# Performance work log

Measured on AMD Instinct MI355X. Metric: run time of the kernel, lower is better.

The kernel has to match this reference:

```python
import jax, jax.numpy as jnp
import numpy as np

B, S = 2, 2048
DIM_IN, DIM_OUT, NUM_HEADS, DIM_QK = 1024, 128, 16, 128


def setup_inputs() -> dict:
    key = jax.random.key(0)
    k0, k1, k2, k3 = jax.random.split(key, 4)
    x = jax.random.normal(k0, (B, S, DIM_IN), jnp.float32)
    mask = jax.random.bernoulli(k1, 0.1, (B, S))  # True = masked-out token
    # xavier-normal-ish scales (exact init values are irrelevant for correctness)
    std_in = float(np.sqrt(2.0 / (NUM_HEADS * DIM_QK + DIM_IN * DIM_QK)))
    proj_in = jax.random.normal(k2, (DIM_IN, NUM_HEADS, 2 * DIM_QK + DIM_OUT), jnp.float32) * std_in
    v_bias = jnp.zeros((NUM_HEADS, DIM_OUT), jnp.float32)
    std_out = float(np.sqrt(2.0 / (DIM_OUT * DIM_OUT + NUM_HEADS * DIM_OUT)))
    proj_out = jax.random.normal(k3, (NUM_HEADS, DIM_OUT, DIM_OUT), jnp.float32) * std_out
    proj_out_bias = jnp.zeros((DIM_OUT,), jnp.float32)
    return {"x": x, "mask": mask, "proj_in": proj_in, "v_bias": v_bias,
            "proj_out": proj_out, "proj_out_bias": proj_out_bias}


def _rotary(t):
    # t: [z, s, h, d]; GPT-NeoX style rotary as in the torch Rotary module
    d = t.shape[-1]
    half = -(-d // 2)  # ceil(d/2), matches torch.arange(0,-1,-2/d)
    freq_half = 10000.0 ** (jnp.arange(half, dtype=jnp.float32) * (-2.0 / d))
    freq = jnp.concatenate([freq_half, freq_half[: half - d % 2]])  # length d
    pos = jnp.arange(t.shape[1], dtype=jnp.float32)
    ang = pos[:, None] * freq[None, :]             # [s, d]
    cos = jnp.cos(ang)[None, :, None, :]
    sin = jnp.sin(ang)[None, :, None, :]
    x1, x2 = jnp.split(t, 2, axis=-1)
    rot = jnp.concatenate([-x2, x1], axis=-1)
    return t * cos + rot * sin


def _inf_cube(t):
    return t ** 3


def reference(x, mask, proj_in, v_bias, proj_out, proj_out_bias):
    qkv = jnp.einsum('zki,iho->zkho', x, proj_in)
    q, k, v = jnp.split(qkv, [DIM_QK, 2 * DIM_QK], axis=-1)
    q = _rotary(q)
    k = _rotary(k)
    scores = jnp.einsum('zqha,zkha->zqkh', q, k) / jnp.sqrt(jnp.float32(DIM_QK))
    # dual mask: row (query) OR column (key) masked -> -inf
    m = jnp.logical_or(mask[:, :, None, None], mask[:, None, :, None])  # [z,q,k,1]
    scores = jnp.where(m, -jnp.inf, scores)
    attn = jnp.nan_to_num(jax.nn.softmax(scores, axis=2))  # softmax over k; nan rows -> 0
    o = jnp.einsum('zqkh,zkhx->zqhx', attn, v + v_bias[None, None])
    out = jnp.einsum('zqhx,hxy->zqy', _inf_cube(o), proj_out) + proj_out_bias[None, None]
    return _inf_cube(out)
```

## Files before the change

### kernel.cpp

```cpp
#include <hip/hip_runtime.h>
#include <math.h>

#define BZ 2
#define SQ 2048
#define DIN 1024
#define HH 16
#define NT 6144
#define MROWS 4096
#define KOUT 2048
#define KSPLIT 8

typedef unsigned short u16t;
typedef unsigned int u32t;
typedef __attribute__((ext_vector_type(8))) short bf16x8;
typedef __attribute__((ext_vector_type(4))) float f32x4;

__device__ __forceinline__ float cubef(float x) { return x * x * x; }

__device__ __forceinline__ u16t f2bf(float f) {
    u32t b = __float_as_uint(f);
    b += 0x7FFFu + ((b >> 16) & 1u);
    return (u16t)(b >> 16);
}
__device__ __forceinline__ float bf2f(u16t u) { return __uint_as_float(((u32t)u) << 16); }
__device__ __forceinline__ u32t pk2(float a, float b) {
    return (u32t)f2bf(a) | ((u32t)f2bf(b) << 16);
}

#if __has_builtin(__builtin_amdgcn_exp2f)
#define EXP2(x) __builtin_amdgcn_exp2f(x)
#else
#define EXP2(x) exp2f(x)
#endif

__device__ __forceinline__ void load_lds16(const void* g, void* l) {
    __builtin_amdgcn_global_load_lds((const __attribute__((address_space(1))) void*)g,
                                     (__attribute__((address_space(3))) void*)l, 16, 0, 0);
}

__global__ __launch_bounds__(256) void bf16_x(const float* __restrict__ x,
                                              u16t* __restrict__ xb) {
    const size_t idx = ((size_t)blockIdx.x * 256 + threadIdx.x) * 8;
    float4 f0 = *(const float4*)&x[idx];
    float4 f1 = *(const float4*)&x[idx + 4];
    u32t h[4];
    h[0] = pk2(f0.x, f0.y); h[1] = pk2(f0.z, f0.w);
    h[2] = pk2(f1.x, f1.y); h[3] = pk2(f1.z, f1.w);
    *(uint4*)&xb[idx] = *(uint4*)&h[0];
}

__global__ __launch_bounds__(256) void rope_table(float* __restrict__ tab) {
    const int idx = blockIdx.x * 256 + threadIdx.x;
    const int s = idx >> 6, d = idx & 63;
    float f = expf(-0.14391156831212788f * (float)d);
    float sn, cs;
    sincosf((float)s * f, &sn, &cs);
    ((float2*)tab)[idx] = make_float2(cs, sn);
}

__global__ __launch_bounds__(256) void transpose_w(const float* __restrict__ W,
                                                   u16t* __restrict__ Th) {
    __shared__ float tile[64][68];
    const int n0 = blockIdx.x * 64;
    const int k0 = blockIdx.y * 64;
    const int t = threadIdx.x;
    {
        const int r = t >> 4, c = (t & 15) * 4;
        #pragma unroll
        for (int p = 0; p < 4; p++) {
            float4 v = *(const float4*)&W[(size_t)(k0 + r + p * 16) * NT + n0 + c];
            *(float4*)&tile[r + p * 16][c] = v;
        }
    }
    __syncthreads();
    const int nr = t >> 2;
    const int kc = (t & 3) * 16;
    u32t hi[8];
    #pragma unroll
    for (int j = 0; j < 8; j++)
        hi[j] = pk2(tile[kc + 2 * j][nr], tile[kc + 2 * j + 1][nr]);
    size_t ob = (size_t)(n0 + nr) * DIN + k0 + kc;
    *(uint4*)&Th[ob]     = *(uint4*)&hi[0];
    *(uint4*)&Th[ob + 8] = *(uint4*)&hi[4];
}

__global__ __launch_bounds__(256) void transpose_w2(const float* __restrict__ W,
                                                    u16t* __restrict__ Th) {
    __shared__ float tile[64][68];
    const int n0 = blockIdx.x * 64;
    const int k0 = blockIdx.y * 64;
    const int t = threadIdx.x;
    {
        const int r = t >> 4, c = (t & 15) * 4;
        #pragma unroll
        for (int p = 0; p < 4; p++) {
            float4 v = *(const float4*)&W[(size_t)(k0 + r + p * 16) * 128 + n0 + c];
            *(float4*)&tile[r + p * 16][c] = v;
        }
    }
    __syncthreads();
    const int nr = t >> 2;
    const int kc = (t & 3) * 16;
    u32t hi[8];
    #pragma unroll
    for (int j = 0; j < 8; j++)
        hi[j] = pk2(tile[kc + 2 * j][nr], tile[kc + 2 * j + 1][nr]);
    size_t ob = (size_t)(n0 + nr) * KOUT + k0 + kc;
    *(uint4*)&Th[ob]     = *(uint4*)&hi[0];
    *(uint4*)&Th[ob + 8] = *(uint4*)&hi[4];
}

#define QSC 0.12751744f

#define GQ_STAGE(TI) do {                                                  \
    const int _k0 = (TI) * 32;                                             \
    const int _bb = ((TI) & 3) * 8192;                                     \
    load_lds16(aPtr + _k0,     &smem[_bb + wbase]);                        \
    load_lds16(aPtr + _k0 + 8, &smem[_bb + wbase + 1024]);                 \
    load_lds16(bPtr + _k0,     &smem[_bb + 4096 + wbase]);                 \
    load_lds16(bPtr + _k0 + 8, &smem[_bb + 4096 + wbase + 1024]);          \
} while (0)

#define GQ_COMPUTE(TI) do {                                                \
    const int _bb = ((TI) & 3) * 8192;                                     \
    bf16x8 ah[4], bh[4];                                                   \
    _Pragma("unroll")                                                      \
    for (int mt = 0; mt < 4; mt++)                                         \
        ah[mt] = *(const bf16x8*)&smem[_bb + quad * 1024 + (wm + mt * 16 + l15) * 8]; \
    _Pragma("unroll")                                                      \
    for (int nt = 0; nt < 4; nt++)                                         \
        bh[nt] = *(const bf16x8*)&smem[_bb + 4096 + quad * 1024 + (wn + nt * 16 + l15) * 8]; \
    __builtin_amdgcn_s_setprio(1);                                         \
    _Pragma("unroll")                                                      \
    for (int mt = 0; mt < 4; mt++)                                         \
        _Pragma("unroll")                                                  \
        for (int nt = 0; nt < 4; nt++)                                     \
            acc[mt][nt] = __builtin_amdgcn_mfma_f32_16x16x32_bf16(ah[mt], bh[nt], acc[mt][nt], 0, 0, 0); \
    __builtin_amdgcn_s_setprio(0);                                         \
} while (0)

#define GQ_WAITBAR(N) do {                                                 \
    asm volatile("s_waitcnt vmcnt(" #N ")" ::: "memory");                  \
    __builtin_amdgcn_s_barrier();                                          \
    __builtin_amdgcn_sched_barrier(0);                                     \
} while (0)

__global__ __launch_bounds__(256, 2) void gemm_qkv6(const u16t* __restrict__ Ah,
                                                    const u16t* __restrict__ Bh,
                                                    const float* __restrict__ vb,
                                                    const float* __restrict__ ropetab,
                                                    u16t* __restrict__ QB,
                                                    u16t* __restrict__ KB,
                                                    u16t* __restrict__ VTh) {
    __shared__ __align__(16) u16t smem[32768];

    const int t = threadIdx.x;
    const int lane = t & 63, wid = t >> 6;
    const int quad = lane >> 4, l15 = lane & 15;
    const int wm = (wid & 1) * 64;
    const int wn = (wid >> 1) * 64;

    const int f = blockIdx.y * 48 + blockIdx.x;
    const int L = (f & 7) * 192 + (f >> 3);
    const int rect = L / 48, rrem = L - rect * 48;
    const int tileI = (rect & 7) * 6 + rrem % 6;
    const int rowIdx = (rect >> 3) * 8 + rrem / 6;
    const int h = tileI / 3, t3 = tileI - h * 3;
    const int colBase = tileI * 128;
    const int rowBase = rowIdx * 128;
    const int sm = t & 127;
    const int skh = t >> 7;

    f32x4 acc[4][4];
    #pragma unroll
    for (int i = 0; i < 4; i++)
        #pragma unroll
        for (int j = 0; j < 4; j++) acc[i][j] = (f32x4){0.f, 0.f, 0.f, 0.f};

    const u16t* aPtr = Ah + (size_t)(rowBase + sm) * DIN + skh * 16;
    const u16t* bPtr = Bh + (size_t)(colBase + sm) * DIN + skh * 16;
    const int wbase = (wid >> 1) * 2048 + (wid & 1) * 512;

    GQ_STAGE(0);
    GQ_STAGE(1);
    for (int i = 0; i < 30; i++) {
        GQ_STAGE(i + 2);
        GQ_WAITBAR(8);
        GQ_COMPUTE(i);
    }
    GQ_WAITBAR(4);
    GQ_COMPUTE(30);
    GQ_WAITBAR(0);
    GQ_COMPUTE(31);
    __syncthreads();

    const int z = rowBase >> 11;
    const int s0local = rowBase & 2047;
    const size_t zh = (size_t)(z * 16 + h);
    u16t* tl = smem;

    if (t3 == 2) {
        #pragma unroll
        for (int nt = 0; nt < 4; nt++) {
            float bbv = vb[h * 128 + wn + nt * 16 + l15];
            #pragma unroll
            for (int mt = 0; mt < 4; mt++)
                #pragma unroll
                for (int r = 0; r < 4; r++)
                    tl[(wm + mt * 16 + quad * 4 + r) * 136 + wn + nt * 16 + l15] =
                        f2bf(acc[mt][nt][r] + bbv);
        }
    } else {
        #pragma unroll
        for (int nt = 0; nt < 4; nt++)
            #pragma unroll
            for (int mt = 0; mt < 4; mt++)
                #pragma unroll
                for (int r = 0; r < 4; r++)
                    tl[(wm + mt * 16 + quad * 4 + r) * 136 + wn + nt * 16 + l15] =
                        f2bf(acc[mt][nt][r]);
    }
    __syncthreads();

    if (t3 != 2) {
        u16t* dstQK = (t3 ? KB : QB) + zh * 262144;
        const float sc = t3 ? 1.0f : QSC;
        const int rr = t >> 2;
        const int ch = (t & 3) << 4;
        #pragma unroll
        for (int half = 0; half < 2; half++) {
            const int row = rr + half * 64;
            const int s = s0local + row;
            const u16t* trow = &tl[row * 136];
            uint4 X1  = *(const uint4*)&trow[ch];
            uint4 X1b = *(const uint4*)&trow[ch + 8];
            uint4 X2  = *(const uint4*)&trow[ch + 64];
            uint4 X2b = *(const uint4*)&trow[ch + 72];
            u32t A_[8] = {X1.x, X1.y, X1.z, X1.w, X1b.x, X1b.y, X1b.z, X1b.w};
            u32t B_[8] = {X2.x, X2.y, X2.z, X2.w, X2b.x, X2b.y, X2b.z, X2b.w};
            u32t OA[8], OB[8];
            const float4* tb = (const float4*)&ropetab[(size_t)s * 128 + ch * 2];
            #pragma unroll
            for (int p = 0; p < 8; p++) {
                float4 tt = tb[p];
                float cs0 = tt.x * sc, sn0 = tt.y * sc;
                float cs1 = tt.z * sc, sn1 = tt.w * sc;
                float x1a = bf2f((u16t)(A_[p] & 0xFFFFu)), x1b = bf2f((u16t)(A_[p] >> 16));
                float x2a = bf2f((u16t)(B_[p] & 0xFFFFu)), x2b = bf2f((u16t)(B_[p] >> 16));
                OA[p] = pk2(x1a * cs0 - x2a * sn0, x1b * cs1 - x2b * sn1);
                OB[p] = pk2(x2a * cs0 + x1a * sn0, x2b * cs1 + x1b * sn1);
            }
            u16t* d0 = dstQK + (size_t)s * 128 + ch;
            *(uint4*)d0        = make_uint4(OA[0], OA[1], OA[2], OA[3]);
            *(uint4*)(d0 + 8)  = make_uint4(OA[4], OA[5], OA[6], OA[7]);
            *(uint4*)(d0 + 64) = make_uint4(OB[0], OB[1], OB[2], OB[3]);
            *(uint4*)(d0 + 72) = make_uint4(OB[4], OB[5], OB[6], OB[7]);
        }
    } else {
        u16t* dstV = VTh + zh * 262144 + (size_t)(s0local >> 5) * 4096;
        const int d = t & 127;
        const int g0 = t >> 7;
        #pragma unroll
        for (int gg = 0; gg < 2; gg++) {
            const int g = g0 + 2 * gg;
            const u16t* col = &tl[(g * 32) * 136 + d];
            u32t H[16];
            #pragma unroll
            for (int m = 0; m < 16; m++) {
                u32t lo = col[m * 136];
                u32t hi = col[(m + 16) * 136];
                H[m] = lo | (hi << 16);
            }
            u16t* dv = dstV + (size_t)g * 4096 + d * 32;
            *(uint4*)&dv[0]  = *(uint4*)&H[0];
            *(uint4*)&dv[8]  = *(uint4*)&H[4];
            *(uint4*)&dv[16] = *(uint4*)&H[8];
            *(uint4*)&dv[24] = *(uint4*)&H[12];
        }
    }
}

__global__ __launch_bounds__(256, 2) void attn_kernel9(const u16t* __restrict__ QB,
                                                       const u16t* __restrict__ KB,
                                                       const u16t* __restrict__ VTh,
                                                       const int* __restrict__ mask,
                                                       u16t* __restrict__ O3b) {
    const int blk = blockIdx.x;
    const int qt = blk & 15;
    const int h  = (blk >> 4) & 15;
    const int z  = blk >> 8;
    const int t  = threadIdx.x;
    const int lane = t & 63, wid = t >> 6;
    const int quad = lane >> 4, l15 = lane & 15;

    __shared__ __align__(16) u16t ks[2][32 * 136];
    __shared__ __align__(16) u16t vth[2][128 * 40];
    __shared__ __align__(16) u16t wlb[128 * 40];
    __shared__ int km[2][32];

    const int q0 = qt * 128;
    const size_t zh = (size_t)(z * 16 + h);
    const u16t* qb  = QB  + zh * 262144;
    const u16t* kb  = KB  + zh * 262144;
    const u16t* vhg = VTh + zh * 262144;

    bf16x8 qf[2][4];
    #pragma unroll
    for (int i = 0; i < 2; i++)
        #pragma unroll
        for (int kk = 0; kk < 4; kk++)
            qf[i][kk] = *(const bf16x8*)(qb + (size_t)(q0 + 16 * (2 * wid + i) + l15) * 128 + kk * 32 + quad * 8);

    int4 qm4[2];
    #pragma unroll
    for (int i = 0; i < 2; i++)
        qm4[i] = *(const int4*)&mask[z * SQ + q0 + 16 * (2 * wid + i) + 4 * quad];
    const int qmr[2][4] = {{qm4[0].x, qm4[0].y, qm4[0].z, qm4[0].w},
                           {qm4[1].x, qm4[1].y, qm4[1].z, qm4[1].w}};
    int rowoff[2];
    #pragma unroll
    for (int i = 0; i < 2; i++) rowoff[i] = (16 * (2 * wid + i) + 4 * quad) * 40;

    const int srow = t >> 3, sco = (t & 7) * 16;
    const int sdd = t >> 1, sk0 = (t & 1) * 16;

    uint4 ka, kb2, va, vb2;
    int kmv = 0;
    {
        ka  = *(const uint4*)(kb + t * 16);
        kb2 = *(const uint4*)(kb + t * 16 + 8);
        va  = *(const uint4*)(vhg + t * 16);
        vb2 = *(const uint4*)(vhg + t * 16 + 8);
        if (t < 32) kmv = mask[z * SQ + t];
    }

    f32x4 acc[2][8];
    #pragma unroll
    for (int i = 0; i < 2; i++)
        #pragma unroll
        for (int d = 0; d < 8; d++) acc[i][d] = (f32x4){0.f, 0.f, 0.f, 0.f};
    float dsum[2][4] = {{0.f, 0.f, 0.f, 0.f}, {0.f, 0.f, 0.f, 0.f}};

    for (int it = 0; it < 64; it++) {
        const int buf = it & 1;
        *(uint4*)&ks[buf][srow * 136 + sco]     = ka;
        *(uint4*)&ks[buf][srow * 136 + sco + 8] = kb2;
        *(uint4*)&vth[buf][sdd * 40 + sk0]      = va;
        *(uint4*)&vth[buf][sdd * 40 + sk0 + 8]  = vb2;
        if (t < 32) km[buf][t] = kmv;

        __syncthreads();

        {
            const int ktn = (it < 63) ? (it + 1) * 32 : it * 32;
            const u16t* src = kb + (size_t)ktn * 128 + t * 16;
            ka  = *(const uint4*)(src);
            kb2 = *(const uint4*)(src + 8);
            const u16t* srch = vhg + (size_t)(ktn >> 5) * 4096 + t * 16;
            va  = *(const uint4*)(srch);
            vb2 = *(const uint4*)(srch + 8);
            if (t < 32) kmv = mask[z * SQ + ktn + t];
        }

        f32x4 s4[2][2];
        #pragma unroll
        for (int i = 0; i < 2; i++)
            #pragma unroll
            for (int n = 0; n < 2; n++) s4[i][n] = (f32x4){0.f, 0.f, 0.f, 0.f};
        __builtin_amdgcn_s_setprio(1);
        #pragma unroll
        for (int kk = 0; kk < 4; kk++) {
            bf16x8 kf0 = *(const bf16x8*)&ks[buf][l15 * 136 + kk * 32 + quad * 8];
            bf16x8 kf1 = *(const bf16x8*)&ks[buf][(16 + l15) * 136 + kk * 32 + quad * 8];
            s4[0][0] = __builtin_amdgcn_mfma_f32_16x16x32_bf16(qf[0][kk], kf0, s4[0][0], 0, 0, 0);
            s4[0][1] = __builtin_amdgcn_mfma_f32_16x16x32_bf16(qf[0][kk], kf1, s4[0][1], 0, 0, 0);
            s4[1][0] = __builtin_amdgcn_mfma_f32_16x16x32_bf16(qf[1][kk], kf0, s4[1][0], 0, 0, 0);
            s4[1][1] = __builtin_amdgcn_mfma_f32_16x16x32_bf16(qf[1][kk], kf1, s4[1][1], 0, 0, 0);
        }
        __builtin_amdgcn_s_setprio(0);
        {
            int colm0 = km[buf][l15], colm1 = km[buf][16 + l15];
            #pragma unroll
            for (int i = 0; i < 2; i++)
                #pragma unroll
                for (int r = 0; r < 4; r++) {
                    float w0 = colm0 ? 0.f : EXP2(s4[i][0][r]);
                    float w1 = colm1 ? 0.f : EXP2(s4[i][1][r]);
                    dsum[i][r] += w0 + w1;
                    u32t pkw;
                    asm("v_cvt_pk_bf16_f32 %0, %1, %2" : "=v"(pkw) : "v"(w0), "v"(w1));
                    *(u32t*)&wlb[rowoff[i] + r * 40 + 2 * l15] = pkw;
                }
        }
        bf16x8 pa[2];
        #pragma unroll
        for (int i = 0; i < 2; i++)
            pa[i] = *(const bf16x8*)&wlb[(16 * (2 * wid + i) + l15) * 40 + quad * 8];
        __builtin_amdgcn_s_setprio(1);
        #pragma unroll
        for (int dt = 0; dt < 8; dt++) {
            bf16x8 vh = *(const bf16x8*)&vth[buf][(16 * dt + l15) * 40 + quad * 8];
            acc[0][dt] = __builtin_amdgcn_mfma_f32_16x16x32_bf16(pa[0], vh, acc[0][dt], 0, 0, 0);
            acc[1][dt] = __builtin_amdgcn_mfma_f32_16x16x32_bf16(pa[1], vh, acc[1][dt], 0, 0, 0);
        }
        __builtin_amdgcn_s_setprio(0);
    }

    #pragma unroll
    for (int i = 0; i < 2; i++)
        #pragma unroll
        for (int r = 0; r < 4; r++) {
            float v = dsum[i][r];
            v += __shfl_xor(v, 1);
            v += __shfl_xor(v, 2);
            v += __shfl_xor(v, 4);
            v += __shfl_xor(v, 8);
            dsum[i][r] = v;
        }

    #pragma unroll
    for (int i = 0; i < 2; i++)
        #pragma unroll
        for (int r = 0; r < 4; r++) {
            int row = 16 * (2 * wid + i) + 4 * quad + r;
            float inv = (qmr[i][r] || !(dsum[i][r] > 0.f)) ? 0.f : 1.f / dsum[i][r];
            u16t* dst = O3b + (size_t)(z * SQ + q0 + row) * KOUT + h * 128;
            #pragma unroll
            for (int dt = 0; dt < 8; dt++)
                dst[16 * dt + l15] = f2bf(cubef(acc[i][dt][r] * inv));
        }
}

__global__ __launch_bounds__(256, 2) void final_gemm4(const u16t* __restrict__ Ab,
                                                      const u16t* __restrict__ Bh,
                                                      float* __restrict__ part) {
    __shared__ __align__(16) u16t smem[32768];

    const int t = threadIdx.x;
    const int lane = t & 63, wid = t >> 6;
    const int quad = lane >> 4, l15 = lane & 15;
    const int wm = (wid & 1) * 64;
    const int wn = (wid >> 1) * 64;
    const int rowBase = blockIdx.x * 128;
    const int kBase   = blockIdx.y * (KOUT / KSPLIT);
    const int sm = t & 127;
    const int skh = t >> 7;

    f32x4 acc[4][4];
    #pragma unroll
    for (int i = 0; i < 4; i++)
        #pragma unroll
        for (int j = 0; j < 4; j++) acc[i][j] = (f32x4){0.f, 0.f, 0.f, 0.f};

    const u16t* aPtr = Ab + (size_t)(rowBase + sm) * KOUT + kBase + skh * 16;
    const u16t* bPtr = Bh + (size_t)sm * KOUT + kBase + skh * 16;
    const int wbase = (wid >> 1) * 2048 + (wid & 1) * 512;

    GQ_STAGE(0);
    GQ_STAGE(1);
    for (int i = 0; i < 6; i++) {
        GQ_STAGE(i + 2);
        GQ_WAITBAR(8);
        GQ_COMPUTE(i);
    }
    GQ_WAITBAR(4);
    GQ_COMPUTE(6);
    GQ_WAITBAR(0);
    GQ_COMPUTE(7);

    float* pbase = part + (size_t)blockIdx.y * ((size_t)MROWS * 128);
    #pragma unroll
    for (int mt = 0; mt < 4; mt++)
        #pragma unroll
        for (int nt = 0; nt < 4; nt++) {
            int col = wn + nt * 16 + l15;
            #pragma unroll
            for (int r = 0; r < 4; r++) {
                int row = rowBase + wm + mt * 16 + quad * 4 + r;
                pbase[(size_t)row * 128 + col] = acc[mt][nt][r];
            }
        }
}

__global__ __launch_bounds__(256) void reduce_bias_cube(const float* __restrict__ part,
                                                        const float* __restrict__ bias,
                                                        float* __restrict__ out) {
    const int idx = (blockIdx.x * 256 + threadIdx.x) * 4;
    float4 s = {0.f, 0.f, 0.f, 0.f};
    #pragma unroll
    for (int p = 0; p < KSPLIT; p++) {
        float4 v = *(const float4*)&part[(size_t)p * ((size_t)MROWS * 128) + idx];
        s.x += v.x; s.y += v.y; s.z += v.z; s.w += v.w;
    }
    float4 b = *(const float4*)&bias[idx & 127];
    float4 r;
    r.x = cubef(s.x + b.x);
    r.y = cubef(s.y + b.y);
    r.z = cubef(s.z + b.z);
    r.w = cubef(s.w + b.w);
    *(float4*)&out[idx] = r;
}

extern "C" void kernel_launch(void* const* d_in, const int* in_sizes, int n_in,
                              void* d_out, int out_size, void* d_ws, size_t ws_size,
                              hipStream_t stream) {
    const float* x        = (const float*)d_in[0];
    const int*   mask     = (const int*)d_in[1];
    const float* proj_in  = (const float*)d_in[2];
    const float* v_bias   = (const float*)d_in[3];
    const float* proj_out = (const float*)d_in[4];
    const float* po_bias  = (const float*)d_in[5];
    float* out = (float*)d_out;

    u16t* QB  = (u16t*)d_ws;
    u16t* KB  = QB + (size_t)8388608;
    u16t* VTh = KB + (size_t)8388608;
    u16t* xb  = VTh + (size_t)8388608;
    u16t* O3b = xb + (size_t)4194304;
    u16t* pTh = O3b;
    float* ropetab = (float*)(O3b + (size_t)6291456);
    u16t* WTh = QB;
    float* partials = (float*)(WTh + (size_t)128 * KOUT);

    bf16_x<<<(MROWS * DIN) / (256 * 8), 256, 0, stream>>>(x, xb);
    rope_table<<<(SQ * 64) / 256, 256, 0, stream>>>(ropetab);
    transpose_w<<<dim3(NT / 64, DIN / 64), 256, 0, stream>>>(proj_in, pTh);
    gemm_qkv6<<<dim3(48, MROWS / 128), 256, 0, stream>>>(xb, pTh, v_bias, ropetab, QB, KB, VTh);
    attn_kernel9<<<BZ * HH * (SQ / 128), 256, 0, stream>>>(QB, KB, VTh, mask, O3b);
    transpose_w2<<<dim3(2, KOUT / 64), 256, 0, stream>>>(proj_out, WTh);
    final_gemm4<<<dim3(MROWS / 128, KSPLIT), 256, 0, stream>>>(O3b, WTh, partials);
    reduce_bias_cube<<<(MROWS * 128) / (256 * 4), 256, 0, stream>>>(partials, po_bias, out);
}
```

Baseline: 300.6 us.

## Merge prep kernels into one launch and use register-prefetch QKV GEMM

Three preprocessing kernels (x to bf16, rope table, proj_in transpose) become a single launch that picks its branch by block index, removing two launch gaps. The QKV GEMM moves from a 4-stage global_load_lds pipeline with a 64 KB LDS footprint to a simpler double-buffered version. That version prefetches the next K-tile into registers, stores it to LDS and syncs once per step, using about 34 KB of LDS with no explicit occupancy hint. The attention kernel is only moved within the file. This risks losing the deeper async-copy overlap of the old GEMM in exchange for lower LDS use and fewer launches.

```diff
diff --git a/kernel.cpp b/kernel.cpp
--- a/kernel.cpp
+++ b/kernel.cpp
@@ -38,50 +38,53 @@
                                      (__attribute__((address_space(3))) void*)l, 16, 0, 0);
 }
 
-__global__ __launch_bounds__(256) void bf16_x(const float* __restrict__ x,
-                                              u16t* __restrict__ xb) {
-    const size_t idx = ((size_t)blockIdx.x * 256 + threadIdx.x) * 8;
-    float4 f0 = *(const float4*)&x[idx];
-    float4 f1 = *(const float4*)&x[idx + 4];
-    u32t h[4];
-    h[0] = pk2(f0.x, f0.y); h[1] = pk2(f0.z, f0.w);
-    h[2] = pk2(f1.x, f1.y); h[3] = pk2(f1.z, f1.w);
-    *(uint4*)&xb[idx] = *(uint4*)&h[0];
-}
-
-__global__ __launch_bounds__(256) void rope_table(float* __restrict__ tab) {
-    const int idx = blockIdx.x * 256 + threadIdx.x;
-    const int s = idx >> 6, d = idx & 63;
-    float f = expf(-0.14391156831212788f * (float)d);
-    float sn, cs;
-    sincosf((float)s * f, &sn, &cs);
-    ((float2*)tab)[idx] = make_float2(cs, sn);
-}
-
-__global__ __launch_bounds__(256) void transpose_w(const float* __restrict__ W,
-                                                   u16t* __restrict__ Th) {
+__global__ __launch_bounds__(256) void prep_all(const float* __restrict__ x,
+                                                u16t* __restrict__ xb,
+                                                float* __restrict__ tab,
+                                                const float* __restrict__ W,
+                                                u16t* __restrict__ Th) {
     __shared__ float tile[64][68];
-    const int n0 = blockIdx.x * 64;
-    const int k0 = blockIdx.y * 64;
+    const int bx = blockIdx.x;
     const int t = threadIdx.x;
-    {
-        const int r = t >> 4, c = (t & 15) * 4;
-        #pragma unroll
-        for (int p = 0; p < 4; p++) {
-            float4 v = *(const float4*)&W[(size_t)(k0 + r + p * 16) * NT + n0 + c];
-            *(float4*)&tile[r + p * 16][c] = v;
-        }
-    }
-    __syncthreads();
-    const int nr = t >> 2;
-    const int kc = (t & 3) * 16;
-    u32t hi[8];
-    #pragma unroll
-    for (int j = 0; j < 8; j++)
-        hi[j] = pk2(tile[kc + 2 * j][nr], tile[kc + 2 * j + 1][nr]);
-    size_t ob = (size_t)(n0 + nr) * DIN + k0 + kc;
-    *(uint4*)&Th[ob]     = *(uint4*)&hi[0];
-    *(uint4*)&Th[ob + 8] = *(uint4*)&hi[4];
+
+    if (bx < 2048) {
+        const size_t idx = ((size_t)bx * 256 + t) * 8;
+        float4 f0 = *(const float4*)&x[idx];
+        float4 f1 = *(const float4*)&x[idx + 4];
+        u32t h[4];
+        h[0] = pk2(f0.x, f0.y); h[1] = pk2(f0.z, f0.w);
+        h[2] = pk2(f1.x, f1.y); h[3] = pk2(f1.z, f1.w);
+        *(uint4*)&xb[idx] = *(uint4*)&h[0];
+    } else if (bx < 2560) {
+        const int idx = (bx - 2048) * 256 + t;
+        const int s = idx >> 6, d = idx & 63;
+        float f = expf(-0.14391156831212788f * (float)d);
+        float sn, cs;
+        sincosf((float)s * f, &sn, &cs);
+        ((float2*)tab)[idx] = make_float2(cs, sn);
+    } else {
+        const int idx = bx - 2560;
+        const int n0 = (idx % 96) * 64;
+        const int k0 = (idx / 96) * 64;
+        {
+            const int r = t >> 4, c = (t & 15) * 4;
+            #pragma unroll
+            for (int p = 0; p < 4; p++) {
+                float4 v = *(const float4*)&W[(size_t)(k0 + r + p * 16) * NT + n0 + c];
+                *(float4*)&tile[r + p * 16][c] = v;
+            }
+        }
+        __syncthreads();
+        const int nr = t >> 2;
+        const int kc = (t & 3) * 16;
+        u32t hi[8];
+        #pragma unroll
+        for (int j = 0; j < 8; j++)
+            hi[j] = pk2(tile[kc + 2 * j][nr], tile[kc + 2 * j + 1][nr]);
+        size_t ob = (size_t)(n0 + nr) * DIN + k0 + kc;
+        *(uint4*)&Th[ob]     = *(uint4*)&hi[0];
+        *(uint4*)&Th[ob + 8] = *(uint4*)&hi[4];
+    }
 }
 
 __global__ __launch_bounds__(256) void transpose_w2(const float* __restrict__ W,
@@ -111,6 +114,322 @@
 }
 
 #define QSC 0.12751744f
+
+__global__ __launch_bounds__(256) void gemm_qkv9(const u16t* __restrict__ Ah,
+                                                 const u16t* __restrict__ Bh,
+                                                 const float* __restrict__ vb,
+                                                 const float* __restrict__ ropetab,
+                                                 u16t* __restrict__ QB,
+                                                 u16t* __restrict__ KB,
+                                                 u16t* __restrict__ VTh) {
+    __shared__ __align__(16) u16t smem[17408];
+
+    const int t = threadIdx.x;
+    const int lane = t & 63, wid = t >> 6;
+    const int quad = lane >> 4, l15 = lane & 15;
+    const int wm = (wid & 1) * 64;
+    const int wn = (wid >> 1) * 64;
+
+    const int f = blockIdx.y * 48 + blockIdx.x;
+    const int L = (f & 7) * 192 + (f >> 3);
+    const int rect = L / 48, rrem = L - rect * 48;
+    const int tileI = (rect & 7) * 6 + rrem % 6;
+    const int rowIdx = (rect >> 3) * 8 + rrem / 6;
+    const int h = tileI / 3, t3 = tileI - h * 3;
+    const int colBase = tileI * 128;
+    const int rowBase = rowIdx * 128;
+    const int sm = t & 127;
+    const int skh = t >> 7;
+
+    f32x4 acc[4][4];
+    #pragma unroll
+    for (int i = 0; i < 4; i++)
+        #pragma unroll
+        for (int j = 0; j < 4; j++) acc[i][j] = (f32x4){0.f, 0.f, 0.f, 0.f};
+
+    const u16t* aPtr = Ah + (size_t)(rowBase + sm) * DIN + skh * 16;
+    const u16t* bPtr = Bh + (size_t)(colBase + sm) * DIN + skh * 16;
+    const int swoff = skh * 2048 + sm * 8;
+
+    uint4 a0 = *(const uint4*)(aPtr);
+    uint4 a1 = *(const uint4*)(aPtr + 8);
+    uint4 b0 = *(const uint4*)(bPtr);
+    uint4 b1 = *(const uint4*)(bPtr + 8);
+
+    for (int it = 0; it < 32; it++) {
+        const int buf = it & 1;
+        const int ab = buf * 4096, bb_ = 8192 + buf * 4096;
+        *(uint4*)(&smem[ab + swoff])         = a0;
+        *(uint4*)(&smem[ab + swoff + 1024])  = a1;
+        *(uint4*)(&smem[bb_ + swoff])        = b0;
+        *(uint4*)(&smem[bb_ + swoff + 1024]) = b1;
+        __syncthreads();
+        {
+            const int k0 = (it < 31) ? (it + 1) * 32 : it * 32;
+            a0 = *(const uint4*)(aPtr + k0);
+            a1 = *(const uint4*)(aPtr + k0 + 8);
+            b0 = *(const uint4*)(bPtr + k0);
+            b1 = *(const uint4*)(bPtr + k0 + 8);
+        }
+        bf16x8 ah[4], bh[4];
+        #pragma unroll
+        for (int mt = 0; mt < 4; mt++)
+            ah[mt] = *(const bf16x8*)&smem[ab + quad * 1024 + (wm + mt * 16 + l15) * 8];
+        #pragma unroll
+        for (int nt = 0; nt < 4; nt++)
+            bh[nt] = *(const bf16x8*)&smem[bb_ + quad * 1024 + (wn + nt * 16 + l15) * 8];
+        __builtin_amdgcn_s_setprio(1);
+        #pragma unroll
+        for (int mt = 0; mt < 4; mt++)
+            #pragma unroll
+            for (int nt = 0; nt < 4; nt++)
+                acc[mt][nt] = __builtin_amdgcn_mfma_f32_16x16x32_bf16(ah[mt], bh[nt], acc[mt][nt], 0, 0, 0);
+        __builtin_amdgcn_s_setprio(0);
+    }
+    __syncthreads();
+
+    const int z = rowBase >> 11;
+    const int s0local = rowBase & 2047;
+    const size_t zh = (size_t)(z * 16 + h);
+    u16t* tl = smem;
+
+    if (t3 == 2) {
+        #pragma unroll
+        for (int nt = 0; nt < 4; nt++) {
+            float bbv = vb[h * 128 + wn + nt * 16 + l15];
+            #pragma unroll
+            for (int mt = 0; mt < 4; mt++)
+                #pragma unroll
+                for (int r = 0; r < 4; r++)
+                    tl[(wm + mt * 16 + quad * 4 + r) * 136 + wn + nt * 16 + l15] =
+                        f2bf(acc[mt][nt][r] + bbv);
+        }
+    } else {
+        #pragma unroll
+        for (int nt = 0; nt < 4; nt++)
+            #pragma unroll
+            for (int mt = 0; mt < 4; mt++)
+                #pragma unroll
+                for (int r = 0; r < 4; r++)
+                    tl[(wm + mt * 16 + quad * 4 + r) * 136 + wn + nt * 16 + l15] =
+                        f2bf(acc[mt][nt][r]);
+    }
+    __syncthreads();
+
+    if (t3 != 2) {
+        u16t* dstQK = (t3 ? KB : QB) + zh * 262144;
+        const float sc = t3 ? 1.0f : QSC;
+        const int rr = t >> 2;
+        const int ch = (t & 3) << 4;
+        #pragma unroll
+        for (int half = 0; half < 2; half++) {
+            const int row = rr + half * 64;
+            const int s = s0local + row;
+            const u16t* trow = &tl[row * 136];
+            uint4 X1  = *(const uint4*)&trow[ch];
+            uint4 X1b = *(const uint4*)&trow[ch + 8];
+            uint4 X2  = *(const uint4*)&trow[ch + 64];
+            uint4 X2b = *(const uint4*)&trow[ch + 72];
+            u32t A_[8] = {X1.x, X1.y, X1.z, X1.w, X1b.x, X1b.y, X1b.z, X1b.w};
+            u32t B_[8] = {X2.x, X2.y, X2.z, X2.w, X2b.x, X2b.y, X2b.z, X2b.w};
+            u32t OA[8], OB[8];
+            const float4* tb = (const float4*)&ropetab[(size_t)s * 128 + ch * 2];
+            #pragma unroll
+            for (int p = 0; p < 8; p++) {
+                float4 tt = tb[p];
+                float cs0 = tt.x * sc, sn0 = tt.y * sc;
+                float cs1 = tt.z * sc, sn1 = tt.w * sc;
+                float x1a = bf2f((u16t)(A_[p] & 0xFFFFu)), x1b = bf2f((u16t)(A_[p] >> 16));
+                float x2a = bf2f((u16t)(B_[p] & 0xFFFFu)), x2b = bf2f((u16t)(B_[p] >> 16));
+                OA[p] = pk2(x1a * cs0 - x2a * sn0, x1b * cs1 - x2b * sn1);
+                OB[p] = pk2(x2a * cs0 + x1a * sn0, x2b * cs1 + x1b * sn1);
+            }
+            u16t* d0 = dstQK + (size_t)s * 128 + ch;
+            *(uint4*)d0        = make_uint4(OA[0], OA[1], OA[2], OA[3]);
+            *(uint4*)(d0 + 8)  = make_uint4(OA[4], OA[5], OA[6], OA[7]);
+            *(uint4*)(d0 + 64) = make_uint4(OB[0], OB[1], OB[2], OB[3]);
+            *(uint4*)(d0 + 72) = make_uint4(OB[4], OB[5], OB[6], OB[7]);
+        }
+    } else {
+        u16t* dstV = VTh + zh * 262144 + (size_t)(s0local >> 5) * 4096;
+        const int d = t & 127;
+        const int g0 = t >> 7;
+        #pragma unroll
+        for (int gg = 0; gg < 2; gg++) {
+            const int g = g0 + 2 * gg;
+            const u16t* col = &tl[(g * 32) * 136 + d];
+            u32t H[16];
+            #pragma unroll
+            for (int m = 0; m < 16; m++) {
+                u32t lo = col[m * 136];
+                u32t hi = col[(m + 16) * 136];
+                H[m] = lo | (hi << 16);
+            }
+            u16t* dv = dstV + (size_t)g * 4096 + d * 32;
+            *(uint4*)&dv[0]  = *(uint4*)&H[0];
+            *(uint4*)&dv[8]  = *(uint4*)&H[4];
+            *(uint4*)&dv[16] = *(uint4*)&H[8];
+            *(uint4*)&dv[24] = *(uint4*)&H[12];
+        }
+    }
+}
+
+__global__ __launch_bounds__(256, 2) void attn_kernel9(const u16t* __restrict__ QB,
+                                                       const u16t* __restrict__ KB,
+                                                       const u16t* __restrict__ VTh,
+                                                       const int* __restrict__ mask,
+                                                       u16t* __restrict__ O3b) {
+    const int blk = blockIdx.x;
+    const int qt = blk & 15;
+    const int h  = (blk >> 4) & 15;
+    const int z  = blk >> 8;
+    const int t  = threadIdx.x;
+    const int lane = t & 63, wid = t >> 6;
+    const int quad = lane >> 4, l15 = lane & 15;
+
+    __shared__ __align__(16) u16t ks[2][32 * 136];
+    __shared__ __align__(16) u16t vth[2][128 * 40];
+    __shared__ __align__(16) u16t wlb[128 * 40];
+    __shared__ int km[2][32];
+
+    const int q0 = qt * 128;
+    const size_t zh = (size_t)(z * 16 + h);
+    const u16t* qb  = QB  + zh * 262144;
+    const u16t* kb  = KB  + zh * 262144;
+    const u16t* vhg = VTh + zh * 262144;
+
+    bf16x8 qf[2][4];
+    #pragma unroll
+    for (int i = 0; i < 2; i++)
+        #pragma unroll
+        for (int kk = 0; kk < 4; kk++)
+            qf[i][kk] = *(const bf16x8*)(qb + (size_t)(q0 + 16 * (2 * wid + i) + l15) * 128 + kk * 32 + quad * 8);
+
+    int4 qm4[2];
+    #pragma unroll
+    for (int i = 0; i < 2; i++)
+        qm4[i] = *(const int4*)&mask[z * SQ + q0 + 16 * (2 * wid + i) + 4 * quad];
+    const int qmr[2][4] = {{qm4[0].x, qm4[0].y, qm4[0].z, qm4[0].w},
+                           {qm4[1].x, qm4[1].y, qm4[1].z, qm4[1].w}};
+    int rowoff[2];
+    #pragma unroll
+    for (int i = 0; i < 2; i++) rowoff[i] = (16 * (2 * wid + i) + 4 * quad) * 40;
+
+    const int srow = t >> 3, sco = (t & 7) * 16;
+    const int sdd = t >> 1, sk0 = (t & 1) * 16;
+
+    uint4 ka, kb2, va, vb2;
+    int kmv = 0;
+    {
+        ka  = *(const uint4*)(kb + t * 16);
+        kb2 = *(const uint4*)(kb + t * 16 + 8);
+        va  = *(const uint4*)(vhg + t * 16);
+        vb2 = *(const uint4*)(vhg + t * 16 + 8);
+        if (t < 32) kmv = mask[z * SQ + t];
+    }
+
+    f32x4 acc[2][8];
+    #pragma unroll
+    for (int i = 0; i < 2; i++)
+        #pragma unroll
+        for (int d = 0; d < 8; d++) acc[i][d] = (f32x4){0.f, 0.f, 0.f, 0.f};
+    float dsum[2][4] = {{0.f, 0.f, 0.f, 0.f}, {0.f, 0.f, 0.f, 0.f}};
+
+    for (int it = 0; it < 64; it++) {
+        const int buf = it & 1;
+        *(uint4*)&ks[buf][srow * 136 + sco]     = ka;
+        *(uint4*)&ks[buf][srow * 136 + sco + 8] = kb2;
+        *(uint4*)&vth[buf][sdd * 40 + sk0]      = va;
+        *(uint4*)&vth[buf][sdd * 40 + sk0 + 8]  = vb2;
+        if (t < 32) km[buf][t] = kmv;
+
+        __syncthreads();
+
+        {
+            const int ktn = (it < 63) ? (it + 1) * 32 : it * 32;
+            const u16t* src = kb + (size_t)ktn * 128 + t * 16;
+            ka  = *(const uint4*)(src);
+            kb2 = *(const uint4*)(src + 8);
+            const u16t* srch = vhg + (size_t)(ktn >> 5) * 4096 + t * 16;
+            va  = *(const uint4*)(srch);
+            vb2 = *(const uint4*)(srch + 8);
+            if (t < 32) kmv = mask[z * SQ + ktn + t];
+        }
+
+        f32x4 s4[2][2];
+        #pragma unroll
+        for (int i = 0; i < 2; i++)
+            #pragma unroll
+            for (int n = 0; n < 2; n++) s4[i][n] = (f32x4){0.f, 0.f, 0.f, 0.f};
+        __builtin_amdgcn_s_setprio(1);
+        #pragma unroll
+        for (int kk = 0; kk < 4; kk++) {
+            bf16x8 kf0 = *(const bf16x8*)&ks[buf][l15 * 136 + kk * 32 + quad * 8];
+            bf16x8 kf1 = *(const bf16x8*)&ks[buf][(16 + l15) * 136 + kk * 32 + quad * 8];
+            s4[0][0] = __builtin_amdgcn_mfma_f32_16x16x32_bf16(qf[0][kk], kf0, s4[0][0], 0, 0, 0);
+            s4[0][1] = __builtin_amdgcn_mfma_f32_16x16x32_bf16(qf[0][kk], kf1, s4[0][1], 0, 0, 0);
+            s4[1][0] = __builtin_amdgcn_mfma_f32_16x16x32_bf16(qf[1][kk], kf0, s4[1][0], 0, 0, 0);
+            s4[1][1] = __builtin_amdgcn_mfma_f32_16x16x32_bf16(qf[1][kk], kf1, s4[1][1], 0, 0, 0);
+        }
+        __builtin_amdgcn_s_setprio(0);
+        {
+            int colm0 = km[buf][l15], colm1 = km[buf][16 + l15];
+            #pragma unroll
+            for (int i = 0; i < 2; i++)
+                #pragma unroll
+                for (int r = 0; r < 4; r++) {
+                    float w0 = colm0 ? 0.f : EXP2(s4[i][0][r]);
+                    float w1 = colm1 ? 0.f : EXP2(s4[i][1][r]);
+                    dsum[i][r] += w0 + w1;
+                    u32t pkw;
+                    asm("v_cvt_pk_bf16_f32 %0, %1, %2" : "=v"(pkw) : "v"(w0), "v"(w1));
+                    *(u32t*)&wlb[rowoff[i] + r * 40 + 2 * l15] = pkw;
+                }
+        }
+        bf16x8 pa[2];
+        #pragma unroll
+        for (int i = 0; i < 2; i++)
+            pa[i] = *(const bf16x8*)&wlb[(16 * (2 * wid + i) + l15) * 40 + quad * 8];
+        __builtin_amdgcn_s_setprio(1);
+        #pragma unroll
+        for (int dt = 0; dt < 8; dt++) {
+            bf16x8 vh = *(const bf16x8*)&vth[buf][(16 * dt + l15) * 40 + quad * 8];
+            acc[0][dt] = __builtin_amdgcn_mfma_f32_16x16x32_bf16(pa[0], vh, acc[0][dt], 0, 0, 0);
+            acc[1][dt] = __builtin_amdgcn_mfma_f32_16x16x32_bf16(pa[1], vh, acc[1][dt], 0, 0, 0);
+        }
+        __builtin_amdgcn_s_setprio(0);
+    }
+
+    #pragma unroll
+    for (int i = 0; i < 2; i++)
+        #pragma unroll
+        for (int r = 0; r < 4; r++) {
+            float v = dsum[i][r];
+            v += __shfl_xor(v, 1);
+            v += __shfl_xor(v, 2);
+            v += __shfl_xor(v, 4);
+            v += __shfl_xor(v, 8);
+            dsum[i][r] = v;
+        }
+
+    #pragma unroll
+    for (int i = 0; i < 2; i++)
+        #pragma unroll
+        for (int r = 0; r < 4; r++) {
+            int row = 16 * (2 * wid + i) + 4 * quad + r;
+            float inv = (qmr[i][r] || !(dsum[i][r] > 0.f)) ? 0.f : 1.f / dsum[i][r];
+            u16t* dst = O3b + (size_t)(z * SQ + q0 + row) * KOUT + h * 128;
+            #pragma unroll
+            for (int dt = 0; dt < 8; dt++)
+                dst[16 * dt + l15] = f2bf(cubef(acc[i][dt][r] * inv));
+        }
+}
+
+#define GQ_WAITBAR(N) do {                                                 \
+    asm volatile("s_waitcnt vmcnt(" #N ")" ::: "memory");                  \
+    __builtin_amdgcn_s_barrier();                                          \
+    __builtin_amdgcn_sched_barrier(0);                                     \
+} while (0)
 
 #define GQ_STAGE(TI) do {                                                  \
     const int _k0 = (TI) * 32;                                             \
@@ -139,298 +458,6 @@
     __builtin_amdgcn_s_setprio(0);                                         \
 } while (0)
 
-#define GQ_WAITBAR(N) do {                                                 \
-    asm volatile("s_waitcnt vmcnt(" #N ")" ::: "memory");                  \
-    __builtin_amdgcn_s_barrier();                                          \
-    __builtin_amdgcn_sched_barrier(0);                                     \
-} while (0)
-
-__global__ __launch_bounds__(256, 2) void gemm_qkv6(const u16t* __restrict__ Ah,
-                                                    const u16t* __restrict__ Bh,
-                                                    const float* __restrict__ vb,
-                                                    const float* __restrict__ ropetab,
-                                                    u16t* __restrict__ QB,
-                                                    u16t* __restrict__ KB,
-                                                    u16t* __restrict__ VTh) {
-    __shared__ __align__(16) u16t smem[32768];
-
-    const int t = threadIdx.x;
-    const int lane = t & 63, wid = t >> 6;
-    const int quad = lane >> 4, l15 = lane & 15;
-    const int wm = (wid & 1) * 64;
-    const int wn = (wid >> 1) * 64;
-
-    const int f = blockIdx.y * 48 + blockIdx.x;
-    const int L = (f & 7) * 192 + (f >> 3);
-    const int rect = L / 48, rrem = L - rect * 48;
-    const int tileI = (rect & 7) * 6 + rrem % 6;
-    const int rowIdx = (rect >> 3) * 8 + rrem / 6;
-    const int h = tileI / 3, t3 = tileI - h * 3;
-    const int colBase = tileI * 128;
-    const int rowBase = rowIdx * 128;
-    const int sm = t & 127;
-    const int skh = t >> 7;
-
-    f32x4 acc[4][4];
-    #pragma unroll
-    for (int i = 0; i < 4; i++)
-        #pragma unroll
-        for (int j = 0; j < 4; j++) acc[i][j] = (f32x4){0.f, 0.f, 0.f, 0.f};
-
-    const u16t* aPtr = Ah + (size_t)(rowBase + sm) * DIN + skh * 16;
-    const u16t* bPtr = Bh + (size_t)(colBase + sm) * DIN + skh * 16;
-    const int wbase = (wid >> 1) * 2048 + (wid & 1) * 512;
-
-    GQ_STAGE(0);
-    GQ_STAGE(1);
-    for (int i = 0; i < 30; i++) {
-        GQ_STAGE(i + 2);
-        GQ_WAITBAR(8);
-        GQ_COMPUTE(i);
-    }
-    GQ_WAITBAR(4);
-    GQ_COMPUTE(30);
-    GQ_WAITBAR(0);
-    GQ_COMPUTE(31);
-    __syncthreads();
-
-    const int z = rowBase >> 11;
-    const int s0local = rowBase & 2047;
-    const size_t zh = (size_t)(z * 16 + h);
-    u16t* tl = smem;
-
-    if (t3 == 2) {
-        #pragma unroll
-        for (int nt = 0; nt < 4; nt++) {
-            float bbv = vb[h * 128 + wn + nt * 16 + l15];
-            #pragma unroll
-            for (int mt = 0; mt < 4; mt++)
-                #pragma unroll
-                for (int r = 0; r < 4; r++)
-                    tl[(wm + mt * 16 + quad * 4 + r) * 136 + wn + nt * 16 + l15] =
-                        f2bf(acc[mt][nt][r] + bbv);
-        }
-    } else {
-        #pragma unroll
-        for (int nt = 0; nt < 4; nt++)
-            #pragma unroll
-            for (int mt = 0; mt < 4; mt++)
-                #pragma unroll
-                for (int r = 0; r < 4; r++)
-                    tl[(wm + mt * 16 + quad * 4 + r) * 136 + wn + nt * 16 + l15] =
-                        f2bf(acc[mt][nt][r]);
-    }
-    __syncthreads();
-
-    if (t3 != 2) {
-        u16t* dstQK = (t3 ? KB : QB) + zh * 262144;
-        const float sc = t3 ? 1.0f : QSC;
-        const int rr = t >> 2;
-        const int ch = (t & 3) << 4;
-        #pragma unroll
-        for (int half = 0; half < 2; half++) {
-            const int row = rr + half * 64;
-            const int s = s0local + row;
-            const u16t* trow = &tl[row * 136];
-            uint4 X1  = *(const uint4*)&trow[ch];
-            uint4 X1b = *(const uint4*)&trow[ch + 8];
-            uint4 X2  = *(const uint4*)&trow[ch + 64];
-            uint4 X2b = *(const uint4*)&trow[ch + 72];
-            u32t A_[8] = {X1.x, X1.y, X1.z, X1.w, X1b.x, X1b.y, X1b.z, X1b.w};
-            u32t B_[8] = {X2.x, X2.y, X2.z, X2.w, X2b.x, X2b.y, X2b.z, X2b.w};
-            u32t OA[8], OB[8];
-            const float4* tb = (const float4*)&ropetab[(size_t)s * 128 + ch * 2];
-            #pragma unroll
-            for (int p = 0; p < 8; p++) {
-                float4 tt = tb[p];
-                float cs0 = tt.x * sc, sn0 = tt.y * sc;
-                float cs1 = tt.z * sc, sn1 = tt.w * sc;
-                float x1a = bf2f((u16t)(A_[p] & 0xFFFFu)), x1b = bf2f((u16t)(A_[p] >> 16));
-                float x2a = bf2f((u16t)(B_[p] & 0xFFFFu)), x2b = bf2f((u16t)(B_[p] >> 16));
-                OA[p] = pk2(x1a * cs0 - x2a * sn0, x1b * cs1 - x2b * sn1);
-                OB[p] = pk2(x2a * cs0 + x1a * sn0, x2b * cs1 + x1b * sn1);
-            }
-            u16t* d0 = dstQK + (size_t)s * 128 + ch;
-            *(uint4*)d0        = make_uint4(OA[0], OA[1], OA[2], OA[3]);
-            *(uint4*)(d0 + 8)  = make_uint4(OA[4], OA[5], OA[6], OA[7]);
-            *(uint4*)(d0 + 64) = make_uint4(OB[0], OB[1], OB[2], OB[3]);
-            *(uint4*)(d0 + 72) = make_uint4(OB[4], OB[5], OB[6], OB[7]);
-        }
-    } else {
-        u16t* dstV = VTh + zh * 262144 + (size_t)(s0local >> 5) * 4096;
-        const int d = t & 127;
-        const int g0 = t >> 7;
-        #pragma unroll
-        for (int gg = 0; gg < 2; gg++) {
-            const int g = g0 + 2 * gg;
-            const u16t* col = &tl[(g * 32) * 136 + d];
-            u32t H[16];
-            #pragma unroll
-            for (int m = 0; m < 16; m++) {
-                u32t lo = col[m * 136];
-                u32t hi = col[(m + 16) * 136];
-                H[m] = lo | (hi << 16);
-            }
-            u16t* dv = dstV + (size_t)g * 4096 + d * 32;
-            *(uint4*)&dv[0]  = *(uint4*)&H[0];
-            *(uint4*)&dv[8]  = *(uint4*)&H[4];
-            *(uint4*)&dv[16] = *(uint4*)&H[8];
-            *(uint4*)&dv[24] = *(uint4*)&H[12];
-        }
-    }
-}
-
-__global__ __launch_bounds__(256, 2) void attn_kernel9(const u16t* __restrict__ QB,
-                                                       const u16t* __restrict__ KB,
-                                                       const u16t* __restrict__ VTh,
-                                                       const int* __restrict__ mask,
-                                                       u16t* __restrict__ O3b) {
-    const int blk = blockIdx.x;
-    const int qt = blk & 15;
-    const int h  = (blk >> 4) & 15;
-    const int z  = blk >> 8;
-    const int t  = threadIdx.x;
-    const int lane = t & 63, wid = t >> 6;
-    const int quad = lane >> 4, l15 = lane & 15;
-
-    __shared__ __align__(16) u16t ks[2][32 * 136];
-    __shared__ __align__(16) u16t vth[2][128 * 40];
-    __shared__ __align__(16) u16t wlb[128 * 40];
-    __shared__ int km[2][32];
-
-    const int q0 = qt * 128;
-    const size_t zh = (size_t)(z * 16 + h);
-    const u16t* qb  = QB  + zh * 262144;
-    const u16t* kb  = KB  + zh * 262144;
-    const u16t* vhg = VTh + zh * 262144;
-
-    bf16x8 qf[2][4];
-    #pragma unroll
-    for (int i = 0; i < 2; i++)
-        #pragma unroll
-        for (int kk = 0; kk < 4; kk++)
-            qf[i][kk] = *(const bf16x8*)(qb + (size_t)(q0 + 16 * (2 * wid + i) + l15) * 128 + kk * 32 + quad * 8);
-
-    int4 qm4[2];
-    #pragma unroll
-    for (int i = 0; i < 2; i++)
-        qm4[i] = *(const int4*)&mask[z * SQ + q0 + 16 * (2 * wid + i) + 4 * quad];
-    const int qmr[2][4] = {{qm4[0].x, qm4[0].y, qm4[0].z, qm4[0].w},
-                           {qm4[1].x, qm4[1].y, qm4[1].z, qm4[1].w}};
-    int rowoff[2];
-    #pragma unroll
-    for (int i = 0; i < 2; i++) rowoff[i] = (16 * (2 * wid + i) + 4 * quad) * 40;
-
-    const int srow = t >> 3, sco = (t & 7) * 16;
-    const int sdd = t >> 1, sk0 = (t & 1) * 16;
-
-    uint4 ka, kb2, va, vb2;
-    int kmv = 0;
-    {
-        ka  = *(const uint4*)(kb + t * 16);
-        kb2 = *(const uint4*)(kb + t * 16 + 8);
-        va  = *(const uint4*)(vhg + t * 16);
-        vb2 = *(const uint4*)(vhg + t * 16 + 8);
-        if (t < 32) kmv = mask[z * SQ + t];
-    }
-
-    f32x4 acc[2][8];
-    #pragma unroll
-    for (int i = 0; i < 2; i++)
-        #pragma unroll
-        for (int d = 0; d < 8; d++) acc[i][d] = (f32x4){0.f, 0.f, 0.f, 0.f};
-    float dsum[2][4] = {{0.f, 0.f, 0.f, 0.f}, {0.f, 0.f, 0.f, 0.f}};
-
-    for (int it = 0; it < 64; it++) {
-        const int buf = it & 1;
-        *(uint4*)&ks[buf][srow * 136 + sco]     = ka;
-        *(uint4*)&ks[buf][srow * 136 + sco + 8] = kb2;
-        *(uint4*)&vth[buf][sdd * 40 + sk0]      = va;
-        *(uint4*)&vth[buf][sdd * 40 + sk0 + 8]  = vb2;
-        if (t < 32) km[buf][t] = kmv;
-
-        __syncthreads();
-
-        {
-            const int ktn = (it < 63) ? (it + 1) * 32 : it * 32;
-            const u16t* src = kb + (size_t)ktn * 128 + t * 16;
-            ka  = *(const uint4*)(src);
-            kb2 = *(const uint4*)(src + 8);
-            const u16t* srch = vhg + (size_t)(ktn >> 5) * 4096 + t * 16;
-            va  = *(const uint4*)(srch);
-            vb2 = *(const uint4*)(srch + 8);
-            if (t < 32) kmv = mask[z * SQ + ktn + t];
-        }
-
-        f32x4 s4[2][2];
-        #pragma unroll
-        for (int i = 0; i < 2; i++)
-            #pragma unroll
-            for (int n = 0; n < 2; n++) s4[i][n] = (f32x4){0.f, 0.f, 0.f, 0.f};
-        __builtin_amdgcn_s_setprio(1);
-        #pragma unroll
-        for (int kk = 0; kk < 4; kk++) {
-            bf16x8 kf0 = *(const bf16x8*)&ks[buf][l15 * 136 + kk * 32 + quad * 8];
-            bf16x8 kf1 = *(const bf16x8*)&ks[buf][(16 + l15) * 136 + kk * 32 + quad * 8];
-            s4[0][0] = __builtin_amdgcn_mfma_f32_16x16x32_bf16(qf[0][kk], kf0, s4[0][0], 0, 0, 0);
-            s4[0][1] = __builtin_amdgcn_mfma_f32_16x16x32_bf16(qf[0][kk], kf1, s4[0][1], 0, 0, 0);
-            s4[1][0] = __builtin_amdgcn_mfma_f32_16x16x32_bf16(qf[1][kk], kf0, s4[1][0], 0, 0, 0);
-            s4[1][1] = __builtin_amdgcn_mfma_f32_16x16x32_bf16(qf[1][kk], kf1, s4[1][1], 0, 0, 0);
-        }
-        __builtin_amdgcn_s_setprio(0);
-        {
-            int colm0 = km[buf][l15], colm1 = km[buf][16 + l15];
-            #pragma unroll
-            for (int i = 0; i < 2; i++)
-                #pragma unroll
-                for (int r = 0; r < 4; r++) {
-                    float w0 = colm0 ? 0.f : EXP2(s4[i][0][r]);
-                    float w1 = colm1 ? 0.f : EXP2(s4[i][1][r]);
-                    dsum[i][r] += w0 + w1;
-                    u32t pkw;
-                    asm("v_cvt_pk_bf16_f32 %0, %1, %2" : "=v"(pkw) : "v"(w0), "v"(w1));
-                    *(u32t*)&wlb[rowoff[i] + r * 40 + 2 * l15] = pkw;
-                }
-        }
-        bf16x8 pa[2];
-        #pragma unroll
-        for (int i = 0; i < 2; i++)
-            pa[i] = *(const bf16x8*)&wlb[(16 * (2 * wid + i) + l15) * 40 + quad * 8];
-        __builtin_amdgcn_s_setprio(1);
-        #pragma unroll
-        for (int dt = 0; dt < 8; dt++) {
-            bf16x8 vh = *(const bf16x8*)&vth[buf][(16 * dt + l15) * 40 + quad * 8];
-            acc[0][dt] = __builtin_amdgcn_mfma_f32_16x16x32_bf16(pa[0], vh, acc[0][dt], 0, 0, 0);
-            acc[1][dt] = __builtin_amdgcn_mfma_f32_16x16x32_bf16(pa[1], vh, acc[1][dt], 0, 0, 0);
-        }
-        __builtin_amdgcn_s_setprio(0);
-    }
-
-    #pragma unroll
-    for (int i = 0; i < 2; i++)
-        #pragma unroll
-        for (int r = 0; r < 4; r++) {
-            float v = dsum[i][r];
-            v += __shfl_xor(v, 1);
-            v += __shfl_xor(v, 2);
-            v += __shfl_xor(v, 4);
-            v += __shfl_xor(v, 8);
-            dsum[i][r] = v;
-        }
-
-    #pragma unroll
-    for (int i = 0; i < 2; i++)
-        #pragma unroll
-        for (int r = 0; r < 4; r++) {
-            int row = 16 * (2 * wid + i) + 4 * quad + r;
-            float inv = (qmr[i][r] || !(dsum[i][r] > 0.f)) ? 0.f : 1.f / dsum[i][r];
-            u16t* dst = O3b + (size_t)(z * SQ + q0 + row) * KOUT + h * 128;
-            #pragma unroll
-            for (int dt = 0; dt < 8; dt++)
-                dst[16 * dt + l15] = f2bf(cubef(acc[i][dt][r] * inv));
-        }
-}
-
 __global__ __launch_bounds__(256, 2) void final_gemm4(const u16t* __restrict__ Ab,
                                                       const u16t* __restrict__ Bh,
                                                       float* __restrict__ part) {
@@ -522,10 +549,8 @@
     u16t* WTh = QB;
     float* partials = (float*)(WTh + (size_t)128 * KOUT);
 
-    bf16_x<<<(MROWS * DIN) / (256 * 8), 256, 0, stream>>>(x, xb);
-    rope_table<<<(SQ * 64) / 256, 256, 0, stream>>>(ropetab);
-    transpose_w<<<dim3(NT / 64, DIN / 64), 256, 0, stream>>>(proj_in, pTh);
-    gemm_qkv6<<<dim3(48, MROWS / 128), 256, 0, stream>>>(xb, pTh, v_bias, ropetab, QB, KB, VTh);
+    prep_all<<<2048 + 512 + 1536, 256, 0, stream>>>(x, xb, ropetab, proj_in, pTh);
+    gemm_qkv9<<<dim3(48, 32), 256, 0, stream>>>(xb, pTh, v_bias, ropetab, QB, KB, VTh);
     attn_kernel9<<<BZ * HH * (SQ / 128), 256, 0, stream>>>(QB, KB, VTh, mask, O3b);
     transpose_w2<<<dim3(2, KOUT / 64), 256, 0, stream>>>(proj_out, WTh);
     final_gemm4<<<dim3(MROWS / 128, KSPLIT), 256, 0, stream>>>(O3b, WTh, partials);
```

New measurement: 295.6 us. Within noise of the previous version (-1.7%).
